# Performance work log

Hardware: AMD Instinct MI355X
Metric: run time of the kernel (lower is better)

## Reference

```python
import jax, jax.numpy as jnp
import numpy as np

B, C, H, W = 8, 1152, 32, 32
N = H * W


def _skew(t):
    # t: (B,3) -> (B,3,3) skew-symmetric
    z = jnp.zeros_like(t[:, 0])
    return jnp.stack([
        jnp.stack([z, -t[:, 2], t[:, 1]], axis=-1),
        jnp.stack([t[:, 2], z, -t[:, 0]], axis=-1),
        jnp.stack([-t[:, 1], t[:, 0], z], axis=-1),
    ], axis=1)


def _fundamental(K1, K2, R, t):
    E = _skew(t) @ R
    U, S, Vt = jnp.linalg.svd(E)
    S = S.at[:, 2].set(0.0)  # enforce rank-2 essential matrix
    E = U @ (S[:, :, None] * Vt)
    return jnp.linalg.inv(jnp.swapaxes(K2, 1, 2)) @ E @ jnp.linalg.inv(K1)


def setup_inputs() -> dict:
    key = jax.random.key(0)
    k1, k2, k3, k4, k5 = jax.random.split(key, 5)
    f_tar = jax.random.normal(k1, (B, C, H, W), dtype=jnp.float32)
    f_src = jax.random.normal(k2, (B, C, H, W), dtype=jnp.float32)
    # realistic invertible intrinsics: [[fx,0,cx],[0,fy,cy],[0,0,1]]
    def intrinsics(k):
        f = 30.0 + 2.0 * jax.random.uniform(k, (B, 2))
        Kt = jnp.zeros((B, 3, 3))
        Kt = Kt.at[:, 0, 0].set(f[:, 0]).at[:, 1, 1].set(f[:, 1])
        Kt = Kt.at[:, 0, 2].set(W / 2.0).at[:, 1, 2].set(H / 2.0).at[:, 2, 2].set(1.0)
        return Kt.astype(jnp.float32)
    K1 = intrinsics(k3)
    K2 = intrinsics(k4)
    # proper rotation via QR of a random matrix
    ka, kb = jax.random.split(k5)
    Q, Rm = jnp.linalg.qr(jax.random.normal(ka, (B, 3, 3)))
    Q = Q * jnp.sign(jnp.diagonal(Rm, axis1=1, axis2=2))[:, None, :]
    Q = Q * jnp.linalg.det(Q)[:, None, None]  # det = +1
    t = jax.random.normal(kb, (B, 3), dtype=jnp.float32)
    return {"f_tar": f_tar, "f_src": f_src, "K1": K1, "K2": K2,
            "R": Q.astype(jnp.float32), "t": t}


def reference(f_tar, f_src, K1, K2, R, t):
    f_src_flat = f_src.reshape(B, C, N)  # (B,C,N)
    # NOTE: torch code computes A = f_src^T @ f_tar but never uses it (dead code); omitted.

    # homogeneous pixel coords, indexing='ij': x=row index, y=col index
    ix, iy = jnp.meshgrid(jnp.arange(H, dtype=jnp.float32),
                          jnp.arange(W, dtype=jnp.float32), indexing='ij')
    combined = jnp.stack([ix.ravel(), iy.ravel(), jnp.ones(N, jnp.float32)], axis=0)  # (3,N)
    combined = jnp.broadcast_to(combined, (B, 3, N))

    F_mat = _fundamental(K1, K2, R, t)                       # (B,3,3)
    lines = F_mat @ combined                                 # (B,3,N)
    lines = lines / lines[:, 2:3, :]

    ones = jnp.ones((B, 1, N), jnp.float32)
    x0 = jnp.zeros((B, 1, N), jnp.float32)
    y0 = -lines[:, 2:3, :] / lines[:, 1:2, :]
    point_0 = jnp.concatenate([x0, y0, ones], axis=1)        # (B,3,N)
    x1 = jnp.full((B, 1, N), float(W), jnp.float32)
    y1 = -(lines[:, 2:3, :] + lines[:, 0:1, :] * W) / lines[:, 1:2, :]
    point_1 = jnp.concatenate([x1, y1, ones], axis=1)        # (B,3,N)

    # point-to-line distance for every (pixel i, line j) pair -> (B,N,N)
    diff = point_0 - point_1                                 # (B,3,N)
    p = combined[:, :, :, None] - point_0[:, :, None, :]     # (B,3,N,N) via broadcast
    d = diff[:, :, None, :]                                  # (B,3,1,N)
    cross = jnp.stack([
        p[:, 1] * d[:, 2] - p[:, 2] * d[:, 1],
        p[:, 2] * d[:, 0] - p[:, 0] * d[:, 2],
        p[:, 0] * d[:, 1] - p[:, 1] * d[:, 0],
    ], axis=1)                                               # (B,3,N,N)
    cross_norm = jnp.sqrt(jnp.sum(cross * cross, axis=1))    # (B,N,N)
    diff_norm = jnp.linalg.norm(diff, axis=1, keepdims=True) # (B,1,N)
    d_epi = cross_norm / diff_norm                           # (B,N,N)

    thre = 0.1
    weight_map = 1.0 - jax.nn.softmax(5.0 * (d_epi - thre), axis=-1)
    attention_map = jax.nn.softmax(weight_map, axis=1)       # softmax over dim=1, per torch code

    out = jnp.einsum('bij,bjc->bic', attention_map, jnp.swapaxes(f_src_flat, 1, 2))  # (B,N,C)
    return out.reshape(B, C, H, W)
```

## Files before the change

kernel.cpp:

```cpp
#include <hip/hip_runtime.h>
#include <hip/hip_bf16.h>
#include <math.h>

#define Bn 8
#define Cn 1152
#define Hn 32
#define Wn 32
#define Nn 1024

typedef short short8 __attribute__((ext_vector_type(8)));
typedef float f32x4 __attribute__((ext_vector_type(4)));

__device__ float g_rmax[Bn * Nn];
__device__ float g_rsuminv[Bn * Nn];
__device__ float g_csum_part[Bn * 8 * Nn];
__device__ unsigned short g_A[(size_t)Bn * Nn * Nn];
__device__ unsigned short g_fb[(size_t)Bn * Cn * Nn];

__device__ inline unsigned short f2bf(float x) {
    __hip_bfloat16 h = __float2bfloat16(x);
    unsigned short u;
    __builtin_memcpy(&u, &h, 2);
    return u;
}

__device__ inline void inv3(const float* M, float* o) {
    float a = M[0], b = M[1], c = M[2];
    float d = M[3], e = M[4], f = M[5];
    float g = M[6], h = M[7], i = M[8];
    float A0 = (e * i - f * h);
    float A1 = -(d * i - f * g);
    float A2 = (d * h - e * g);
    float det = a * A0 + b * A1 + c * A2;
    float inv = 1.0f / det;
    o[0] = A0 * inv;
    o[1] = -(b * i - c * h) * inv;
    o[2] = (b * f - c * e) * inv;
    o[3] = A1 * inv;
    o[4] = (a * i - c * g) * inv;
    o[5] = -(a * f - c * d) * inv;
    o[6] = A2 * inv;
    o[7] = -(a * h - b * g) * inv;
    o[8] = (a * e - b * d) * inv;
}

__device__ inline void mm3(const float* X, const float* Y, float* Z) {
    for (int r = 0; r < 3; r++)
        for (int c = 0; c < 3; c++)
            Z[r * 3 + c] = X[r * 3 + 0] * Y[0 * 3 + c] + X[r * 3 + 1] * Y[1 * 3 + c] +
                           X[r * 3 + 2] * Y[2 * 3 + c];
}

__device__ inline void computeF(const float* K1, const float* K2, const float* R,
                                const float* t, int b, float* F) {
    float t0 = t[b * 3 + 0], t1 = t[b * 3 + 1], t2 = t[b * 3 + 2];
    float S[9] = {0.0f, -t2, t1, t2, 0.0f, -t0, -t1, t0, 0.0f};
    float E[9];
    mm3(S, &R[b * 9], E);
    float iK1[9], iK2[9];
    inv3(&K1[b * 9], iK1);
    inv3(&K2[b * 9], iK2);
    float iK2T[9] = {iK2[0], iK2[3], iK2[6], iK2[1], iK2[4], iK2[7], iK2[2], iK2[5], iK2[8]};
    float T[9];
    mm3(iK2T, E, T);
    mm3(T, iK1, F);
}

__device__ inline float4 zcoef(const float* F, int j) {
    float jx = (float)(j >> 5);
    float jy = (float)(j & 31);
    float l0 = F[0] * jx + F[1] * jy + F[2];
    float l1 = F[3] * jx + F[4] * jy + F[5];
    float l2 = F[6] * jx + F[7] * jy + F[8];
    l0 = l0 / l2;
    l1 = l1 / l2;
    float y0 = -1.0f / l1;
    float y1 = -(1.0f + l0 * 32.0f) / l1;
    float dy = y0 - y1;
    float invn = 1.0f / sqrtf(1024.0f + dy * dy);
    return make_float4(5.0f * dy * invn, 160.0f * invn, 160.0f * y0 * invn, 0.0f);
}

__global__ void rowstats_kernel(const float* __restrict__ K1, const float* __restrict__ K2,
                                const float* __restrict__ R, const float* __restrict__ t) {
    __shared__ float Fs[9];
    __shared__ float4 prm[Nn];
    int lin = blockIdx.x;
    int b = lin & 7;
    int seg = lin >> 3;
    if (threadIdx.x == 0) computeF(K1, K2, R, t, b, Fs);
    __syncthreads();
#pragma unroll
    for (int u = 0; u < 4; u++) {
        int j = threadIdx.x * 4 + u;
        prm[j] = zcoef(Fs, j);
    }
    __syncthreads();
    int wv = threadIdx.x >> 6;
    int lane = threadIdx.x & 63;
    int i = seg * 4 + wv;
    float ix = (float)(i >> 5), iy = (float)(i & 31);
    float z[16];
    float m = -INFINITY;
#pragma unroll
    for (int k = 0; k < 16; k++) {
        float4 p = prm[lane + k * 64];
        z[k] = fabsf(fmaf(ix, p.x, fmaf(iy, p.y, -p.z))) - 0.5f;
        m = fmaxf(m, z[k]);
    }
#pragma unroll
    for (int o = 32; o > 0; o >>= 1) m = fmaxf(m, __shfl_xor(m, o, 64));
    float s = 0.0f;
#pragma unroll
    for (int k = 0; k < 16; k++) s += __expf(z[k] - m);
#pragma unroll
    for (int o = 32; o > 0; o >>= 1) s += __shfl_xor(s, o, 64);
    if (lane == 0) {
        g_rmax[b * Nn + i] = m;
        g_rsuminv[b * Nn + i] = 1.0f / s;
    }
}

__global__ void colE_kernel(const float* __restrict__ K1, const float* __restrict__ K2,
                            const float* __restrict__ R, const float* __restrict__ t) {
    __shared__ float Fs[9];
    __shared__ float rm[128], rs[128];
    __shared__ float4 red[16][16];
    int lin = blockIdx.x;
    int b = lin & 7;
    int r = lin >> 3;
    int jt = r & 15;
    int it = r >> 4;
    int tt = threadIdx.x;
    if (tt < 128) {
        rm[tt] = g_rmax[b * Nn + it * 128 + tt];
        rs[tt] = g_rsuminv[b * Nn + it * 128 + tt];
    }
    if (tt == 0) computeF(K1, K2, R, t, b, Fs);
    __syncthreads();
    int tcol = tt & 15, trow = tt >> 4;
    int j0 = jt * 64 + tcol * 4;
    float4 p0 = zcoef(Fs, j0 + 0);
    float4 p1 = zcoef(Fs, j0 + 1);
    float4 p2 = zcoef(Fs, j0 + 2);
    float4 p3 = zcoef(Fs, j0 + 3);
    float4 csum = make_float4(0.f, 0.f, 0.f, 0.f);
#pragma unroll
    for (int k = 0; k < 8; k++) {
        int il = trow + k * 16;
        float rmax = rm[il], rsi = rs[il];
        int i = it * 128 + il;
        float ix = (float)(i >> 5), iy = (float)(i & 31);
        float z0 = fabsf(fmaf(ix, p0.x, fmaf(iy, p0.y, -p0.z))) - 0.5f;
        float z1 = fabsf(fmaf(ix, p1.x, fmaf(iy, p1.y, -p1.z))) - 0.5f;
        float z2 = fabsf(fmaf(ix, p2.x, fmaf(iy, p2.y, -p2.z))) - 0.5f;
        float z3 = fabsf(fmaf(ix, p3.x, fmaf(iy, p3.y, -p3.z))) - 0.5f;
        float E0 = __expf(1.0f - __expf(z0 - rmax) * rsi);
        float E1 = __expf(1.0f - __expf(z1 - rmax) * rsi);
        float E2 = __expf(1.0f - __expf(z2 - rmax) * rsi);
        float E3 = __expf(1.0f - __expf(z3 - rmax) * rsi);
        csum.x += E0; csum.y += E1; csum.z += E2; csum.w += E3;
        ushort4 u;
        u.x = f2bf(E0); u.y = f2bf(E1); u.z = f2bf(E2); u.w = f2bf(E3);
        *(ushort4*)&g_A[((size_t)b * Nn + i) * Nn + j0] = u;
    }
    red[trow][tcol] = csum;
    __syncthreads();
    if (tt < 16) {
        float4 s = red[0][tt];
#pragma unroll
        for (int q = 1; q < 16; q++) {
            float4 p = red[q][tt];
            s.x += p.x; s.y += p.y; s.z += p.z; s.w += p.w;
        }
        *(float4*)&g_csum_part[(b * 8 + it) * Nn + jt * 64 + tt * 4] = s;
    }
}

__global__ void convert_fsrc_kernel(const float* __restrict__ f) {
    int lin = blockIdx.x;
    int b = lin & 7;
    int cg = lin >> 3;
    int j0 = threadIdx.x * 4;
    float4 cs = *(const float4*)&g_csum_part[(b * 8 + 0) * Nn + j0];
#pragma unroll
    for (int it = 1; it < 8; it++) {
        float4 p = *(const float4*)&g_csum_part[(b * 8 + it) * Nn + j0];
        cs.x += p.x; cs.y += p.y; cs.z += p.z; cs.w += p.w;
    }
    float4 inv = make_float4(1.0f / cs.x, 1.0f / cs.y, 1.0f / cs.z, 1.0f / cs.w);
#pragma unroll
    for (int c8 = 0; c8 < 8; c8++) {
        int c = cg * 8 + c8;
        size_t off = ((size_t)b * Cn + c) * Nn + j0;
        float4 v = *(const float4*)(f + off);
        ushort4 u;
        u.x = f2bf(v.x * inv.x);
        u.y = f2bf(v.y * inv.y);
        u.z = f2bf(v.z * inv.z);
        u.w = f2bf(v.w * inv.w);
        *(ushort4*)&g_fb[off] = u;
    }
}

#define BM 128
#define BNc 64
#define BK 32

__launch_bounds__(128) __global__ void gemm_kernel(float* __restrict__ out) {
    __shared__ unsigned short As[2][BM * BK];
    __shared__ unsigned short Bs[2][BNc * BK];
    int lin = blockIdx.x;
    int b = lin & 7;
    int s = lin >> 3;
    int it = s & 7;
    int ct = s >> 3;
    int i0 = it * BM;
    int c0 = ct * BNc;
    int t = threadIdx.x;
    int w = t >> 6, L = t & 63;
    const unsigned short* Ab = g_A + (size_t)b * Nn * Nn + (size_t)i0 * Nn;
    const unsigned short* Fb = g_fb + (size_t)b * Cn * Nn + (size_t)c0 * Nn;

    auto stage = [&](int p, int kt) {
#pragma unroll
        for (int h = 0; h < 2; h++) {
            int chunk = h * 128 + t;
            int rr = chunk >> 2;
            int gq = (chunk & 3) ^ ((rr >> 1) & 3);
            const unsigned short* ga = Ab + (size_t)rr * Nn + kt + gq * 8;
            __builtin_amdgcn_global_load_lds(
                (const __attribute__((address_space(1))) unsigned int*)ga,
                (__attribute__((address_space(3))) unsigned int*)(As[p] + chunk * 8), 16, 0, 0);
        }
        {
            int chunk = t;
            int rr = chunk >> 2;
            int gq = (chunk & 3) ^ ((rr >> 1) & 3);
            const unsigned short* gb = Fb + (size_t)rr * Nn + kt + gq * 8;
            __builtin_amdgcn_global_load_lds(
                (const __attribute__((address_space(1))) unsigned int*)gb,
                (__attribute__((address_space(3))) unsigned int*)(Bs[p] + chunk * 8), 16, 0, 0);
        }
    };

    f32x4 acc[4][4] = {};
    int lrow = L & 15, quad = L >> 4;
    auto stage2 = [&](int p, int kt) {
#pragma unroll
        for (int h = 0; h < 4; h++) {
            int chunk = h * 128 + t;
            int rr = chunk >> 2;
            int gq = (chunk & 3) ^ ((rr >> 1) & 3);
            const unsigned short* ga = Ab + (size_t)rr * Nn + kt + gq * 8;
            __builtin_amdgcn_global_load_lds(
                (const __attribute__((address_space(1))) unsigned int*)ga,
                (__attribute__((address_space(3))) unsigned int*)(As[p] + chunk * 8), 16, 0, 0);
        }
#pragma unroll
        for (int h = 0; h < 2; h++) {
            int chunk = h * 128 + t;
            int rr = chunk >> 2;
            int gq = (chunk & 3) ^ ((rr >> 1) & 3);
            const unsigned short* gb = Fb + (size_t)rr * Nn + kt + gq * 8;
            __builtin_amdgcn_global_load_lds(
                (const __attribute__((address_space(1))) unsigned int*)gb,
                (__attribute__((address_space(3))) unsigned int*)(Bs[p] + chunk * 8), 16, 0, 0);
        }
    };
    (void)stage;

    stage2(0, 0);
    for (int kt = 0; kt < Nn; kt += BK) {
        int p = (kt >> 5) & 1;
        __syncthreads();
        if (kt + BK < Nn) stage2(1 - p, kt + BK);
        short8 af[4], bf[4];
#pragma unroll
        for (int mt = 0; mt < 4; mt++) {
            int rr = w * 64 + mt * 16 + lrow;
            int q = quad ^ ((rr >> 1) & 3);
            af[mt] = *(const short8*)(As[p] + rr * BK + q * 8);
        }
#pragma unroll
        for (int nt = 0; nt < 4; nt++) {
            int cc = nt * 16 + lrow;
            int q = quad ^ ((cc >> 1) & 3);
            bf[nt] = *(const short8*)(Bs[p] + cc * BK + q * 8);
        }
#pragma unroll
        for (int mt = 0; mt < 4; mt++)
#pragma unroll
            for (int nt = 0; nt < 4; nt++)
                acc[mt][nt] =
                    __builtin_amdgcn_mfma_f32_16x16x32_bf16(af[mt], bf[nt], acc[mt][nt], 0, 0, 0);
    }
    int col = L & 15;
#pragma unroll
    for (int mt = 0; mt < 4; mt++)
#pragma unroll
        for (int rg = 0; rg < 4; rg++) {
            int i = i0 + w * 64 + mt * 16 + quad * 4 + rg;
            float* orow = out + ((size_t)b * Nn + i) * Cn + c0;
#pragma unroll
            for (int nt = 0; nt < 4; nt++) orow[nt * 16 + col] = acc[mt][nt][rg];
        }
}

extern "C" void kernel_launch(void* const* d_in, const int* in_sizes, int n_in,
                              void* d_out, int out_size, void* d_ws, size_t ws_size,
                              hipStream_t stream) {
    (void)in_sizes; (void)n_in; (void)d_ws; (void)ws_size; (void)out_size;
    const float* f_src = (const float*)d_in[1];
    const float* K1 = (const float*)d_in[2];
    const float* K2 = (const float*)d_in[3];
    const float* R = (const float*)d_in[4];
    const float* t = (const float*)d_in[5];
    float* out = (float*)d_out;

    rowstats_kernel<<<dim3(2048), dim3(256), 0, stream>>>(K1, K2, R, t);
    colE_kernel<<<dim3(1024), dim3(256), 0, stream>>>(K1, K2, R, t);
    convert_fsrc_kernel<<<dim3(Bn * Cn / 8), dim3(256), 0, stream>>>(f_src);
    gemm_kernel<<<dim3(Bn * (Nn / BM) * (Cn / BNc)), dim3(128), 0, stream>>>(out);
}
```

Before: 171.4 us.

## Fuse all stages into one persistent kernel with per-batch grid barriers

Replaces the four launches (row stats, column exp/A write, f_src conversion, GEMM) with a single kernel of 1152 blocks. Per-batch atomic spin barriers in workspace separate the phases. Row stats are now computed per block for its own 8 rows, so the separate row-stats pass and its global round-trip go away. Column partial sums grow to 128 partials per batch, and every block re-reduces all of them. This removes launch gaps and tail effects between stages, but it relies on every block of a batch being co-resident and adds spin-wait and redundant reduction cost.

```diff
diff --git a/kernel.cpp b/kernel.cpp
--- a/kernel.cpp
+++ b/kernel.cpp
@@ -4,16 +4,13 @@
 
 #define Bn 8
 #define Cn 1152
-#define Hn 32
-#define Wn 32
 #define Nn 1024
+#define NBPB 144
 
 typedef short short8 __attribute__((ext_vector_type(8)));
 typedef float f32x4 __attribute__((ext_vector_type(4)));
 
-__device__ float g_rmax[Bn * Nn];
-__device__ float g_rsuminv[Bn * Nn];
-__device__ float g_csum_part[Bn * 8 * Nn];
+__device__ float g_csum_part[Bn * 128 * Nn];
 __device__ unsigned short g_A[(size_t)Bn * Nn * Nn];
 __device__ unsigned short g_fb[(size_t)Bn * Cn * Nn];
 
@@ -81,245 +78,219 @@
     return make_float4(5.0f * dy * invn, 160.0f * invn, 160.0f * y0 * invn, 0.0f);
 }
 
-__global__ void rowstats_kernel(const float* __restrict__ K1, const float* __restrict__ K2,
-                                const float* __restrict__ R, const float* __restrict__ t) {
-    __shared__ float Fs[9];
-    __shared__ float4 prm[Nn];
-    int lin = blockIdx.x;
-    int b = lin & 7;
-    int seg = lin >> 3;
-    if (threadIdx.x == 0) computeF(K1, K2, R, t, b, Fs);
+__device__ inline void batch_barrier(unsigned int* bar, int b, int ph) {
     __syncthreads();
-#pragma unroll
-    for (int u = 0; u < 4; u++) {
-        int j = threadIdx.x * 4 + u;
-        prm[j] = zcoef(Fs, j);
+    if (threadIdx.x == 0) {
+        __threadfence();
+        atomicAdd(&bar[ph * 8 + b], 1u);
+        while (__hip_atomic_load(&bar[ph * 8 + b], __ATOMIC_RELAXED,
+                                 __HIP_MEMORY_SCOPE_AGENT) < (unsigned)NBPB)
+            __builtin_amdgcn_s_sleep(2);
+        __threadfence();
     }
     __syncthreads();
-    int wv = threadIdx.x >> 6;
-    int lane = threadIdx.x & 63;
-    int i = seg * 4 + wv;
-    float ix = (float)(i >> 5), iy = (float)(i & 31);
-    float z[16];
-    float m = -INFINITY;
-#pragma unroll
-    for (int k = 0; k < 16; k++) {
-        float4 p = prm[lane + k * 64];
-        z[k] = fabsf(fmaf(ix, p.x, fmaf(iy, p.y, -p.z))) - 0.5f;
-        m = fmaxf(m, z[k]);
-    }
-#pragma unroll
-    for (int o = 32; o > 0; o >>= 1) m = fmaxf(m, __shfl_xor(m, o, 64));
-    float s = 0.0f;
-#pragma unroll
-    for (int k = 0; k < 16; k++) s += __expf(z[k] - m);
-#pragma unroll
-    for (int o = 32; o > 0; o >>= 1) s += __shfl_xor(s, o, 64);
-    if (lane == 0) {
-        g_rmax[b * Nn + i] = m;
-        g_rsuminv[b * Nn + i] = 1.0f / s;
-    }
-}
-
-__global__ void colE_kernel(const float* __restrict__ K1, const float* __restrict__ K2,
-                            const float* __restrict__ R, const float* __restrict__ t) {
-    __shared__ float Fs[9];
-    __shared__ float rm[128], rs[128];
-    __shared__ float4 red[16][16];
-    int lin = blockIdx.x;
-    int b = lin & 7;
-    int r = lin >> 3;
-    int jt = r & 15;
-    int it = r >> 4;
-    int tt = threadIdx.x;
-    if (tt < 128) {
-        rm[tt] = g_rmax[b * Nn + it * 128 + tt];
-        rs[tt] = g_rsuminv[b * Nn + it * 128 + tt];
-    }
-    if (tt == 0) computeF(K1, K2, R, t, b, Fs);
-    __syncthreads();
-    int tcol = tt & 15, trow = tt >> 4;
-    int j0 = jt * 64 + tcol * 4;
-    float4 p0 = zcoef(Fs, j0 + 0);
-    float4 p1 = zcoef(Fs, j0 + 1);
-    float4 p2 = zcoef(Fs, j0 + 2);
-    float4 p3 = zcoef(Fs, j0 + 3);
-    float4 csum = make_float4(0.f, 0.f, 0.f, 0.f);
-#pragma unroll
-    for (int k = 0; k < 8; k++) {
-        int il = trow + k * 16;
-        float rmax = rm[il], rsi = rs[il];
-        int i = it * 128 + il;
-        float ix = (float)(i >> 5), iy = (float)(i & 31);
-        float z0 = fabsf(fmaf(ix, p0.x, fmaf(iy, p0.y, -p0.z))) - 0.5f;
-        float z1 = fabsf(fmaf(ix, p1.x, fmaf(iy, p1.y, -p1.z))) - 0.5f;
-        float z2 = fabsf(fmaf(ix, p2.x, fmaf(iy, p2.y, -p2.z))) - 0.5f;
-        float z3 = fabsf(fmaf(ix, p3.x, fmaf(iy, p3.y, -p3.z))) - 0.5f;
-        float E0 = __expf(1.0f - __expf(z0 - rmax) * rsi);
-        float E1 = __expf(1.0f - __expf(z1 - rmax) * rsi);
-        float E2 = __expf(1.0f - __expf(z2 - rmax) * rsi);
-        float E3 = __expf(1.0f - __expf(z3 - rmax) * rsi);
-        csum.x += E0; csum.y += E1; csum.z += E2; csum.w += E3;
-        ushort4 u;
-        u.x = f2bf(E0); u.y = f2bf(E1); u.z = f2bf(E2); u.w = f2bf(E3);
-        *(ushort4*)&g_A[((size_t)b * Nn + i) * Nn + j0] = u;
-    }
-    red[trow][tcol] = csum;
-    __syncthreads();
-    if (tt < 16) {
-        float4 s = red[0][tt];
-#pragma unroll
-        for (int q = 1; q < 16; q++) {
-            float4 p = red[q][tt];
-            s.x += p.x; s.y += p.y; s.z += p.z; s.w += p.w;
-        }
-        *(float4*)&g_csum_part[(b * 8 + it) * Nn + jt * 64 + tt * 4] = s;
-    }
-}
-
-__global__ void convert_fsrc_kernel(const float* __restrict__ f) {
-    int lin = blockIdx.x;
-    int b = lin & 7;
-    int cg = lin >> 3;
-    int j0 = threadIdx.x * 4;
-    float4 cs = *(const float4*)&g_csum_part[(b * 8 + 0) * Nn + j0];
-#pragma unroll
-    for (int it = 1; it < 8; it++) {
-        float4 p = *(const float4*)&g_csum_part[(b * 8 + it) * Nn + j0];
-        cs.x += p.x; cs.y += p.y; cs.z += p.z; cs.w += p.w;
-    }
-    float4 inv = make_float4(1.0f / cs.x, 1.0f / cs.y, 1.0f / cs.z, 1.0f / cs.w);
-#pragma unroll
-    for (int c8 = 0; c8 < 8; c8++) {
-        int c = cg * 8 + c8;
-        size_t off = ((size_t)b * Cn + c) * Nn + j0;
-        float4 v = *(const float4*)(f + off);
-        ushort4 u;
-        u.x = f2bf(v.x * inv.x);
-        u.y = f2bf(v.y * inv.y);
-        u.z = f2bf(v.z * inv.z);
-        u.w = f2bf(v.w * inv.w);
-        *(ushort4*)&g_fb[off] = u;
-    }
 }
 
 #define BM 128
 #define BNc 64
 #define BK 32
 
-__launch_bounds__(128) __global__ void gemm_kernel(float* __restrict__ out) {
-    __shared__ unsigned short As[2][BM * BK];
-    __shared__ unsigned short Bs[2][BNc * BK];
+__launch_bounds__(128) __global__
+void fused_kernel(const float* __restrict__ f_src, const float* __restrict__ K1,
+                  const float* __restrict__ K2, const float* __restrict__ Rm,
+                  const float* __restrict__ tv, float* __restrict__ out,
+                  unsigned int* __restrict__ bar) {
+    __shared__ __align__(16) char smem[24576];
+    float4* prm = (float4*)smem;
+    float* rmv = (float*)(smem + 16384);
+    float* rsv = (float*)(smem + 16416);
+    float* Fsh = (float*)(smem + 16448);
+    unsigned short* As0 = (unsigned short*)smem;
+    unsigned short* Bs0 = (unsigned short*)(smem + 16384);
+
     int lin = blockIdx.x;
     int b = lin & 7;
     int s = lin >> 3;
-    int it = s & 7;
-    int ct = s >> 3;
-    int i0 = it * BM;
-    int c0 = ct * BNc;
     int t = threadIdx.x;
-    int w = t >> 6, L = t & 63;
-    const unsigned short* Ab = g_A + (size_t)b * Nn * Nn + (size_t)i0 * Nn;
-    const unsigned short* Fb = g_fb + (size_t)b * Cn * Nn + (size_t)c0 * Nn;
-
-    auto stage = [&](int p, int kt) {
-#pragma unroll
-        for (int h = 0; h < 2; h++) {
-            int chunk = h * 128 + t;
-            int rr = chunk >> 2;
-            int gq = (chunk & 3) ^ ((rr >> 1) & 3);
-            const unsigned short* ga = Ab + (size_t)rr * Nn + kt + gq * 8;
-            __builtin_amdgcn_global_load_lds(
-                (const __attribute__((address_space(1))) unsigned int*)ga,
-                (__attribute__((address_space(3))) unsigned int*)(As[p] + chunk * 8), 16, 0, 0);
-        }
-        {
-            int chunk = t;
-            int rr = chunk >> 2;
-            int gq = (chunk & 3) ^ ((rr >> 1) & 3);
-            const unsigned short* gb = Fb + (size_t)rr * Nn + kt + gq * 8;
-            __builtin_amdgcn_global_load_lds(
-                (const __attribute__((address_space(1))) unsigned int*)gb,
-                (__attribute__((address_space(3))) unsigned int*)(Bs[p] + chunk * 8), 16, 0, 0);
-        }
-    };
-
-    f32x4 acc[4][4] = {};
-    int lrow = L & 15, quad = L >> 4;
-    auto stage2 = [&](int p, int kt) {
-#pragma unroll
-        for (int h = 0; h < 4; h++) {
-            int chunk = h * 128 + t;
-            int rr = chunk >> 2;
-            int gq = (chunk & 3) ^ ((rr >> 1) & 3);
-            const unsigned short* ga = Ab + (size_t)rr * Nn + kt + gq * 8;
-            __builtin_amdgcn_global_load_lds(
-                (const __attribute__((address_space(1))) unsigned int*)ga,
-                (__attribute__((address_space(3))) unsigned int*)(As[p] + chunk * 8), 16, 0, 0);
-        }
-#pragma unroll
-        for (int h = 0; h < 2; h++) {
-            int chunk = h * 128 + t;
-            int rr = chunk >> 2;
-            int gq = (chunk & 3) ^ ((rr >> 1) & 3);
-            const unsigned short* gb = Fb + (size_t)rr * Nn + kt + gq * 8;
-            __builtin_amdgcn_global_load_lds(
-                (const __attribute__((address_space(1))) unsigned int*)gb,
-                (__attribute__((address_space(3))) unsigned int*)(Bs[p] + chunk * 8), 16, 0, 0);
-        }
-    };
-    (void)stage;
-
-    stage2(0, 0);
-    for (int kt = 0; kt < Nn; kt += BK) {
-        int p = (kt >> 5) & 1;
+
+    if (t == 0) computeF(K1, K2, Rm, tv, b, Fsh);
+    __syncthreads();
+
+    if (s < 128) {
+#pragma unroll
+        for (int u = 0; u < 8; u++) {
+            int j = t * 8 + u;
+            prm[j] = zcoef(Fsh, j);
+        }
         __syncthreads();
-        if (kt + BK < Nn) stage2(1 - p, kt + BK);
-        short8 af[4], bf[4];
-#pragma unroll
-        for (int mt = 0; mt < 4; mt++) {
-            int rr = w * 64 + mt * 16 + lrow;
-            int q = quad ^ ((rr >> 1) & 3);
-            af[mt] = *(const short8*)(As[p] + rr * BK + q * 8);
-        }
-#pragma unroll
-        for (int nt = 0; nt < 4; nt++) {
-            int cc = nt * 16 + lrow;
-            int q = quad ^ ((cc >> 1) & 3);
-            bf[nt] = *(const short8*)(Bs[p] + cc * BK + q * 8);
-        }
+        int r0 = s * 8;
+        int wv = t >> 6, lane = t & 63;
+#pragma unroll
+        for (int rr = 0; rr < 4; rr++) {
+            int i = r0 + rr * 2 + wv;
+            float ix = (float)(i >> 5), iy = (float)(i & 31);
+            float z[16], m = -INFINITY;
+#pragma unroll
+            for (int k = 0; k < 16; k++) {
+                float4 p = prm[lane + k * 64];
+                z[k] = fabsf(fmaf(ix, p.x, fmaf(iy, p.y, -p.z))) - 0.5f;
+                m = fmaxf(m, z[k]);
+            }
+#pragma unroll
+            for (int o = 32; o > 0; o >>= 1) m = fmaxf(m, __shfl_xor(m, o, 64));
+            float sm = 0.0f;
+#pragma unroll
+            for (int k = 0; k < 16; k++) sm += __expf(z[k] - m);
+#pragma unroll
+            for (int o = 32; o > 0; o >>= 1) sm += __shfl_xor(sm, o, 64);
+            if (lane == 0) {
+                rmv[rr * 2 + wv] = m;
+                rsv[rr * 2 + wv] = 1.0f / sm;
+            }
+        }
+        __syncthreads();
+        int j0 = t * 8;
+        float4 q[8];
+#pragma unroll
+        for (int u = 0; u < 8; u++) q[u] = prm[j0 + u];
+        float cs[8] = {0.f, 0.f, 0.f, 0.f, 0.f, 0.f, 0.f, 0.f};
+#pragma unroll
+        for (int ii = 0; ii < 8; ii++) {
+            int i = r0 + ii;
+            float rmax = rmv[ii], rsi = rsv[ii];
+            float ix = (float)(i >> 5), iy = (float)(i & 31);
+            short8 ev;
+#pragma unroll
+            for (int u = 0; u < 8; u++) {
+                float z = fabsf(fmaf(ix, q[u].x, fmaf(iy, q[u].y, -q[u].z))) - 0.5f;
+                float E = __expf(1.0f - __expf(z - rmax) * rsi);
+                cs[u] += E;
+                ev[u] = (short)f2bf(E);
+            }
+            *(short8*)&g_A[((size_t)b * Nn + i) * Nn + j0] = ev;
+        }
+        float* cp = &g_csum_part[((size_t)b * 128 + s) * Nn + j0];
+        *(float4*)cp = make_float4(cs[0], cs[1], cs[2], cs[3]);
+        *(float4*)(cp + 4) = make_float4(cs[4], cs[5], cs[6], cs[7]);
+    }
+    batch_barrier(bar, b, 0);
+
+    {
+        int j0 = t * 8;
+        float4 a0 = make_float4(0.f, 0.f, 0.f, 0.f);
+        float4 a1 = make_float4(0.f, 0.f, 0.f, 0.f);
+#pragma unroll 4
+        for (int p = 0; p < 128; p++) {
+            const float* pp = &g_csum_part[((size_t)b * 128 + p) * Nn + j0];
+            float4 v0 = *(const float4*)pp;
+            float4 v1 = *(const float4*)(pp + 4);
+            a0.x += v0.x; a0.y += v0.y; a0.z += v0.z; a0.w += v0.w;
+            a1.x += v1.x; a1.y += v1.y; a1.z += v1.z; a1.w += v1.w;
+        }
+        float inv[8] = {1.0f / a0.x, 1.0f / a0.y, 1.0f / a0.z, 1.0f / a0.w,
+                        1.0f / a1.x, 1.0f / a1.y, 1.0f / a1.z, 1.0f / a1.w};
+#pragma unroll
+        for (int cc = 0; cc < 8; cc++) {
+            int c = s * 8 + cc;
+            size_t off = ((size_t)b * Cn + c) * Nn + j0;
+            float4 v0 = *(const float4*)(f_src + off);
+            float4 v1 = *(const float4*)(f_src + off + 4);
+            short8 u;
+            u[0] = (short)f2bf(v0.x * inv[0]);
+            u[1] = (short)f2bf(v0.y * inv[1]);
+            u[2] = (short)f2bf(v0.z * inv[2]);
+            u[3] = (short)f2bf(v0.w * inv[3]);
+            u[4] = (short)f2bf(v1.x * inv[4]);
+            u[5] = (short)f2bf(v1.y * inv[5]);
+            u[6] = (short)f2bf(v1.z * inv[6]);
+            u[7] = (short)f2bf(v1.w * inv[7]);
+            *(short8*)&g_fb[off] = u;
+        }
+    }
+    batch_barrier(bar, b, 1);
+
+    {
+        int it = s & 7, ct = s >> 3;
+        int i0 = it * BM, c0 = ct * BNc;
+        int w = t >> 6, L = t & 63;
+        const unsigned short* Ab = g_A + (size_t)b * Nn * Nn + (size_t)i0 * Nn;
+        const unsigned short* Fb = g_fb + (size_t)b * Cn * Nn + (size_t)c0 * Nn;
+        auto stage = [&](int p, int kt) {
+#pragma unroll
+            for (int h = 0; h < 4; h++) {
+                int chunk = h * 128 + t;
+                int rr = chunk >> 2;
+                int gq = (chunk & 3) ^ ((rr >> 1) & 3);
+                const unsigned short* ga = Ab + (size_t)rr * Nn + kt + gq * 8;
+                __builtin_amdgcn_global_load_lds(
+                    (const __attribute__((address_space(1))) unsigned int*)ga,
+                    (__attribute__((address_space(3))) unsigned int*)(As0 + p * 4096 + chunk * 8),
+                    16, 0, 0);
+            }
+#pragma unroll
+            for (int h = 0; h < 2; h++) {
+                int chunk = h * 128 + t;
+                int rr = chunk >> 2;
+                int gq = (chunk & 3) ^ ((rr >> 1) & 3);
+                const unsigned short* gb = Fb + (size_t)rr * Nn + kt + gq * 8;
+                __builtin_amdgcn_global_load_lds(
+                    (const __attribute__((address_space(1))) unsigned int*)gb,
+                    (__attribute__((address_space(3))) unsigned int*)(Bs0 + p * 2048 + chunk * 8),
+                    16, 0, 0);
+            }
+        };
+        f32x4 acc[4][4] = {};
+        int lrow = L & 15, quad = L >> 4;
+        stage(0, 0);
+        for (int kt = 0; kt < Nn; kt += BK) {
+            int p = (kt >> 5) & 1;
+            __syncthreads();
+            if (kt + BK < Nn) stage(1 - p, kt + BK);
+            short8 af[4], bf[4];
+#pragma unroll
+            for (int mt = 0; mt < 4; mt++) {
+                int rr = w * 64 + mt * 16 + lrow;
+                int q = quad ^ ((rr >> 1) & 3);
+                af[mt] = *(const short8*)(As0 + p * 4096 + rr * BK + q * 8);
+            }
+#pragma unroll
+            for (int nt = 0; nt < 4; nt++) {
+                int cc = nt * 16 + lrow;
+                int q = quad ^ ((cc >> 1) & 3);
+                bf[nt] = *(const short8*)(Bs0 + p * 2048 + cc * BK + q * 8);
+            }
+#pragma unroll
+            for (int mt = 0; mt < 4; mt++)
+#pragma unroll
+                for (int nt = 0; nt < 4; nt++)
+                    acc[mt][nt] = __builtin_amdgcn_mfma_f32_16x16x32_bf16(af[mt], bf[nt],
+                                                                          acc[mt][nt], 0, 0, 0);
+        }
+        int col = L & 15;
 #pragma unroll
         for (int mt = 0; mt < 4; mt++)
 #pragma unroll
-            for (int nt = 0; nt < 4; nt++)
-                acc[mt][nt] =
-                    __builtin_amdgcn_mfma_f32_16x16x32_bf16(af[mt], bf[nt], acc[mt][nt], 0, 0, 0);
-    }
-    int col = L & 15;
-#pragma unroll
-    for (int mt = 0; mt < 4; mt++)
-#pragma unroll
-        for (int rg = 0; rg < 4; rg++) {
-            int i = i0 + w * 64 + mt * 16 + quad * 4 + rg;
-            float* orow = out + ((size_t)b * Nn + i) * Cn + c0;
-#pragma unroll
-            for (int nt = 0; nt < 4; nt++) orow[nt * 16 + col] = acc[mt][nt][rg];
-        }
+            for (int rg = 0; rg < 4; rg++) {
+                int i = i0 + w * 64 + mt * 16 + quad * 4 + rg;
+                float* orow = out + ((size_t)b * Nn + i) * Cn + c0;
+#pragma unroll
+                for (int nt = 0; nt < 4; nt++) orow[nt * 16 + col] = acc[mt][nt][rg];
+            }
+    }
 }
 
 extern "C" void kernel_launch(void* const* d_in, const int* in_sizes, int n_in,
                               void* d_out, int out_size, void* d_ws, size_t ws_size,
                               hipStream_t stream) {
-    (void)in_sizes; (void)n_in; (void)d_ws; (void)ws_size; (void)out_size;
+    (void)in_sizes; (void)n_in; (void)ws_size; (void)out_size;
     const float* f_src = (const float*)d_in[1];
     const float* K1 = (const float*)d_in[2];
     const float* K2 = (const float*)d_in[3];
     const float* R = (const float*)d_in[4];
     const float* t = (const float*)d_in[5];
     float* out = (float*)d_out;
-
-    rowstats_kernel<<<dim3(2048), dim3(256), 0, stream>>>(K1, K2, R, t);
-    colE_kernel<<<dim3(1024), dim3(256), 0, stream>>>(K1, K2, R, t);
-    convert_fsrc_kernel<<<dim3(Bn * Cn / 8), dim3(256), 0, stream>>>(f_src);
-    gemm_kernel<<<dim3(Bn * (Nn / BM) * (Cn / BNc)), dim3(128), 0, stream>>>(out);
-}
+    unsigned int* bar = (unsigned int*)d_ws;
+
+    hipMemsetAsync(bar, 0, 64, stream);
+    fused_kernel<<<dim3(Bn * NBPB), dim3(128), 0, stream>>>(f_src, K1, K2, R, t, out, bar);
+}
```

Result: slower. 465.7 us (+171.7%).
